# Kernel optimization log

Measured on AMD Instinct MI355X. Metric: run time of the kernel, lower is better.

## Reference

```python
import jax, jax.numpy as jnp
import numpy as np

MAX_ATOMS = 50
N_GRAPH_FEAT = 30
N_ATOM_FEAT = 75
BATCH_SIZE = 128
N_ATOMS = MAX_ATOMS * BATCH_SIZE  # 6400 total padded atoms
HIDDEN = 100
N_INPUTS = N_ATOM_FEAT + (MAX_ATOMS - 1) * N_GRAPH_FEAT  # 1545


def setup_inputs() -> dict:
    key = jax.random.key(0)
    ks = jax.random.split(key, 6)
    atom_features = jax.random.normal(ks[0], (N_ATOMS, N_ATOM_FEAT), dtype=jnp.float32)
    parents = jax.random.randint(ks[1], (N_ATOMS, MAX_ATOMS, MAX_ATOMS), 0, MAX_ATOMS + 1, dtype=jnp.int32)
    calculation_orders = jax.random.randint(ks[2], (N_ATOMS, MAX_ATOMS), 0, N_ATOMS, dtype=jnp.int32)
    calculation_masks = jax.random.randint(ks[3], (N_ATOMS, MAX_ATOMS), 0, 2, dtype=jnp.int32) > 0
    # glorot_uniform weights, zero biases (as in build())
    s0 = float(np.sqrt(6.0 / (N_INPUTS + HIDDEN)))
    W0 = jax.random.uniform(ks[4], (N_INPUTS, HIDDEN), jnp.float32, -s0, s0)
    s1 = float(np.sqrt(6.0 / (HIDDEN + N_GRAPH_FEAT)))
    W1 = jax.random.uniform(ks[5], (HIDDEN, N_GRAPH_FEAT), jnp.float32, -s1, s1)
    b0 = jnp.zeros((HIDDEN,), jnp.float32)
    b1 = jnp.zeros((N_GRAPH_FEAT,), jnp.float32)
    return {
        "atom_features": atom_features,
        "parents": parents,
        "calculation_orders": calculation_orders,
        "calculation_masks": calculation_masks,
        "n_atoms": N_ATOMS,
        "W0": W0, "b0": b0, "W1": W1, "b1": b1,
    }


def reference(atom_features, parents, calculation_orders, calculation_masks, n_atoms, W0, b0, W1, b1):
    # Stateful DAG propagation. Original masks out inactive rows per step
    # (dynamic shapes); here we compute all rows and write back the old value
    # for inactive rows, which is the same math under jit.
    rows = jnp.arange(n_atoms)

    def mlp(x):
        h = jax.nn.relu(x @ W0 + b0)
        return jax.nn.relu(h @ W1 + b1)

    gf0 = jnp.zeros((MAX_ATOMS * BATCH_SIZE, MAX_ATOMS + 1, N_GRAPH_FEAT), jnp.float32)
    # per-step slices, leading axis = count
    xs = (parents.transpose(1, 0, 2),       # [T, N, MAX_ATOMS]
          calculation_orders.T,             # [T, N]
          calculation_masks.T)              # [T, N]

    def step(gf, xs_t):
        par, order, mask = xs_t
        batch_atom = atom_features[order]                     # [N, 75]
        # gather parent graph features: gf[row, parent_slot]
        bgf = gf[rows[:, None], par[:, 1:]]                   # [N, 49, 30]
        x = jnp.concatenate([batch_atom, bgf.reshape(n_atoms, -1)], axis=1)  # [N, 1545]
        out = mlp(x)                                          # [N, 30]
        col = par[:, 0]
        old = gf[rows, col]
        new = jnp.where(mask[:, None], out, old)
        gf = gf.at[rows, col].set(new)
        return gf, out

    _, outs = jax.lax.scan(step, gf0, xs)
    out_last = outs[-1]
    # original returns only the masked rows of the last step; zero out inactive
    return jnp.where(calculation_masks[:, -1][:, None], out_last, 0.0)
```

## Files before the change

kernel.cpp:

```cpp
#include <hip/hip_runtime.h>
#include <stdint.h>

#define MA    50
#define NGF   30
#define NAF   75
#define NA    6400
#define H     100
#define RPB   32
#define NTHR  512
#define NT0P  8
#define KT0   52
#define NT1   2
#define KT1   4
#define AFW   104
#define HHW   136

typedef _Float16 f16;
typedef _Float16 f16x8 __attribute__((ext_vector_type(8)));
typedef float    f32x4 __attribute__((ext_vector_type(4)));

#define MFMA16(a, b, c) __builtin_amdgcn_mfma_f32_16x16x32_f16((a), (b), (c), 0, 0, 0)

__global__ void prep(const float* __restrict__ W0, const float* __restrict__ W1,
                     const uint8_t* __restrict__ cm,
                     f16* __restrict__ w0h, f16* __restrict__ w1h, f16* __restrict__ w1l,
                     int* __restrict__ flag) {
    const int bid = blockIdx.x;
    const int tidb = threadIdx.x;
    if (bid == 0) {
        if (tidb < 64) {
            int any = 0;
            #pragma unroll
            for (int i = 0; i < 64; ++i) {
                int pos = i * 64 + tidb;
                if ((pos & 3) != 0 && cm[pos] != 0) any = 1;
            }
            unsigned long long b = __ballot(any != 0);
            if (tidb == 0) *flag = (b != 0ULL) ? 1 : 0;
        }
        return;
    }
    if (bid <= 104) {
        int idx = (bid - 1) * 256 + tidb;
        int lane = idx & 63;
        int ktn  = idx >> 6;
        int nt = ktn / KT0, kt = ktn % KT0;
        int col = nt * 16 + (lane & 15);
        #pragma unroll
        for (int e = 0; e < 8; ++e) {
            int k = kt * 32 + (lane >> 4) * 8 + e;
            int kr = -1;
            if (kt < 3) { if (k < NAF) kr = k; }
            else {
                int kk = k - kt * 32;
                if (kk < NGF) kr = NAF + (kt - 3) * NGF + kk;
            }
            float wv = (kr >= 0 && col < H) ? W0[(size_t)kr * H + col] : 0.f;
            w0h[(size_t)idx * 8 + e] = (f16)wv;
        }
        return;
    }
    {
        int idx = (bid - 105) * 256 + tidb;
        if (idx >= NT1 * KT1 * 64) return;
        int lane = idx & 63;
        int ktn  = idx >> 6;
        int nt = ktn / KT1, kt = ktn % KT1;
        int col = nt * 16 + (lane & 15);
        #pragma unroll
        for (int e = 0; e < 8; ++e) {
            int k = kt * 32 + (lane >> 4) * 8 + e;
            float wv = (k < H && col < NGF) ? W1[(size_t)k * NGF + col] : 0.f;
            f16 hi = (f16)wv;
            w1h[(size_t)idx * 8 + e] = hi;
            w1l[(size_t)idx * 8 + e] = (f16)((wv - (float)hi) * 1024.f);
        }
    }
}

__global__ __launch_bounds__(NTHR, 2) void dag_mfma(
    const float* __restrict__ af,
    const int*   __restrict__ parents,
    const int*   __restrict__ orders,
    const void*  __restrict__ cmask,
    const float* __restrict__ b0,
    const float* __restrict__ b1,
    const f16*   __restrict__ w0h,
    const f16*   __restrict__ w1h, const f16* __restrict__ w1l,
    const int*   __restrict__ flagp,
    float*       __restrict__ dout)
{
    __shared__ f16     gfh[51 * 1024];
    __shared__ f16     afh[RPB][AFW];
    __shared__ f16     hh[RPB][HHW];
    __shared__ f32x4   part[4][2][2][64];
    __shared__ float   outl[RPB][33];
    __shared__ uint8_t slots[RPB][52];
    __shared__ int     colc[2][RPB];
    __shared__ int     maskc[2][RPB];
    __shared__ int     ordl[2][RPB];

    const int tid   = threadIdx.x;
    const int w     = tid >> 6;
    const int lane  = tid & 63;
    const int mrow  = lane & 15;
    const int kg    = lane >> 4;
    const int npair = w & 3;
    const int half  = w >> 2;
    const int row0  = blockIdx.x * RPB;
    const int flag  = *flagp;

    const int base0 = (mrow * 32 + kg * 8) ^ ((mrow & 7) << 3);
    const int base1 = ((16 + mrow) * 32 + kg * 8) ^ ((mrow & 7) << 3);

    const int hc0 = npair * 32 + mrow;
    const int hc1 = npair * 32 + 16 + mrow;
    const float b0v0 = (w < 4 && hc0 < H) ? b0[hc0] : 0.f;
    const float b0v1 = (w < 4 && hc1 < H) ? b0[hc1] : 0.f;
    const int oc = (w - 4) * 16 + mrow;
    const float b1v = (w >= 4 && w < 6 && oc < NGF) ? b1[oc] : 0.f;

    {
        f16x8 z = 0;
        for (int e = tid; e < 51 * 128; e += NTHR) ((f16x8*)gfh)[e] = z;
        for (int e = tid; e < RPB * AFW / 8; e += NTHR) ((f16x8*)&afh[0][0])[e] = z;
        for (int e = tid; e < RPB * HHW / 8; e += NTHR) ((f16x8*)&hh[0][0])[e]  = z;
    }
    if (tid >= 384 && tid < 416) {
        int r = tid - 384;
        ordl[0][r] = orders[(size_t)(row0 + r) * MA];
    }
    __syncthreads();

    float afr0 = 0.f, afr1 = 0.f, afr2 = 0.f, afr3 = 0.f, afr4 = 0.f;
    int   slr0 = 0, slr1 = 0, slr2 = 0, slr3 = 0;
    int   colr = 0, mskr = 0, oreg = 0;

    auto LOADS = [&](int T) {
        const int* ordb = ordl[T & 1];
        {
            int idx, r, k;
            idx = tid;        r = idx / NAF; k = idx - r * NAF; afr0 = af[(size_t)ordb[r] * NAF + k];
            idx = tid + 512;  r = idx / NAF; k = idx - r * NAF; afr1 = af[(size_t)ordb[r] * NAF + k];
            idx = tid + 1024; r = idx / NAF; k = idx - r * NAF; afr2 = af[(size_t)ordb[r] * NAF + k];
            idx = tid + 1536; r = idx / NAF; k = idx - r * NAF; afr3 = af[(size_t)ordb[r] * NAF + k];
            if (tid < 352) {
                idx = tid + 2048; r = idx / NAF; k = idx - r * NAF;
                afr4 = af[(size_t)ordb[r] * NAF + k];
            }
        }
        {
            int idx, r, p;
            idx = tid;        r = idx / 49; p = idx - r * 49;
            slr0 = __builtin_nontemporal_load(&parents[((size_t)(row0 + r) * MA + T) * MA + 1 + p]);
            idx = tid + 512;  r = idx / 49; p = idx - r * 49;
            slr1 = __builtin_nontemporal_load(&parents[((size_t)(row0 + r) * MA + T) * MA + 1 + p]);
            idx = tid + 1024; r = idx / 49; p = idx - r * 49;
            slr2 = __builtin_nontemporal_load(&parents[((size_t)(row0 + r) * MA + T) * MA + 1 + p]);
            if (tid < 32) {
                idx = tid + 1536; r = idx / 49; p = idx - r * 49;
                slr3 = __builtin_nontemporal_load(&parents[((size_t)(row0 + r) * MA + T) * MA + 1 + p]);
            }
        }
        if (tid >= 416 && tid < 448) {
            int r = tid - 416;
            colr = __builtin_nontemporal_load(&parents[((size_t)(row0 + r) * MA + T) * MA]);
        }
        if (tid >= 448 && tid < 480) {
            int r = tid - 448;
            if (flag) mskr = (int)__builtin_nontemporal_load(&((const uint8_t*)cmask)[(size_t)(row0 + r) * MA + T]);
            else      mskr = __builtin_nontemporal_load(&((const int*)cmask)[(size_t)(row0 + r) * MA + T]);
        }
        if (T + 1 < MA && tid >= 384 && tid < 416) {
            int r = tid - 384;
            oreg = __builtin_nontemporal_load(&orders[(size_t)(row0 + r) * MA + T + 1]);
        }
    };

    LOADS(0);

    for (int t = 0; t < MA; ++t) {
        {
            int idx, r, k;
            idx = tid;        r = idx / NAF; k = idx - r * NAF; afh[r][k] = (f16)afr0;
            idx = tid + 512;  r = idx / NAF; k = idx - r * NAF; afh[r][k] = (f16)afr1;
            idx = tid + 1024; r = idx / NAF; k = idx - r * NAF; afh[r][k] = (f16)afr2;
            idx = tid + 1536; r = idx / NAF; k = idx - r * NAF; afh[r][k] = (f16)afr3;
            if (tid < 352) { idx = tid + 2048; r = idx / NAF; k = idx - r * NAF; afh[r][k] = (f16)afr4; }
        }
        {
            int idx, r, p;
            idx = tid;        r = idx / 49; p = idx - r * 49; slots[r][p] = (uint8_t)slr0;
            idx = tid + 512;  r = idx / 49; p = idx - r * 49; slots[r][p] = (uint8_t)slr1;
            idx = tid + 1024; r = idx / 49; p = idx - r * 49; slots[r][p] = (uint8_t)slr2;
            if (tid < 32) { idx = tid + 1536; r = idx / 49; p = idx - r * 49; slots[r][p] = (uint8_t)slr3; }
        }
        if (tid >= 416 && tid < 448) colc[t & 1][tid - 416]  = colr;
        if (tid >= 448 && tid < 480) maskc[t & 1][tid - 448] = mskr;
        if (t + 1 < MA && tid >= 384 && tid < 416) ordl[(t + 1) & 1][tid - 384] = oreg;
        if (t > 0) {
            const int tp = (t - 1) & 1;
            int e = tid;
            #pragma unroll
            for (int q = 0; q < 2; ++q, e += NTHR) {
                if (e < RPB * NGF) {
                    int r = e / NGF, c = e - r * NGF;
                    float v = outl[r][c];
                    if (maskc[tp][r])
                        gfh[(colc[tp][r] * 1024 + r * 32 + c) ^ ((r & 7) << 3)] = (f16)v;
                }
            }
        }
        __syncthreads();

        if (t + 1 < MA) LOADS(t + 1);

        f32x4 acc00 = {0.f,0.f,0.f,0.f}, acc01 = {0.f,0.f,0.f,0.f};
        f32x4 acc10 = {0.f,0.f,0.f,0.f}, acc11 = {0.f,0.f,0.f,0.f};
        {
            const f16x8* B0 = (const f16x8*)w0h + ((size_t)(2 * npair) * KT0 + half * 26) * 64 + lane;
            const f16x8* B1 = B0 + (size_t)KT0 * 64;
            if (half == 0) {
                #pragma unroll
                for (int kt = 0; kt < 3; ++kt) {
                    f16x8 a0 = *(const f16x8*)&afh[mrow][kt * 32 + kg * 8];
                    f16x8 a1 = *(const f16x8*)&afh[16 + mrow][kt * 32 + kg * 8];
                    f16x8 bb0 = B0[(size_t)kt * 64];
                    f16x8 bb1 = B1[(size_t)kt * 64];
                    acc00 = MFMA16(a0, bb0, acc00); acc10 = MFMA16(a1, bb0, acc10);
                    acc01 = MFMA16(a0, bb1, acc01); acc11 = MFMA16(a1, bb1, acc11);
                }
                #pragma unroll
                for (int g = 0; g < 23; ++g) {
                    int s0 = slots[mrow][g];
                    int s1 = slots[16 + mrow][g];
                    f16x8 a0 = *(const f16x8*)&gfh[s0 * 1024 + base0];
                    f16x8 a1 = *(const f16x8*)&gfh[s1 * 1024 + base1];
                    f16x8 bb0 = B0[(size_t)(3 + g) * 64];
                    f16x8 bb1 = B1[(size_t)(3 + g) * 64];
                    acc00 = MFMA16(a0, bb0, acc00); acc10 = MFMA16(a1, bb0, acc10);
                    acc01 = MFMA16(a0, bb1, acc01); acc11 = MFMA16(a1, bb1, acc11);
                }
            } else {
                #pragma unroll
                for (int g = 0; g < 26; ++g) {
                    int s0 = slots[mrow][23 + g];
                    int s1 = slots[16 + mrow][23 + g];
                    f16x8 a0 = *(const f16x8*)&gfh[s0 * 1024 + base0];
                    f16x8 a1 = *(const f16x8*)&gfh[s1 * 1024 + base1];
                    f16x8 bb0 = B0[(size_t)g * 64];
                    f16x8 bb1 = B1[(size_t)g * 64];
                    acc00 = MFMA16(a0, bb0, acc00); acc10 = MFMA16(a1, bb0, acc10);
                    acc01 = MFMA16(a0, bb1, acc01); acc11 = MFMA16(a1, bb1, acc11);
                }
            }
        }
        if (half) {
            part[npair][0][0][lane] = acc00;
            part[npair][0][1][lane] = acc01;
            part[npair][1][0][lane] = acc10;
            part[npair][1][1][lane] = acc11;
        }
        __syncthreads();

        if (!half) {
            acc00 += part[npair][0][0][lane];
            acc01 += part[npair][0][1][lane];
            acc10 += part[npair][1][0][lane];
            acc11 += part[npair][1][1][lane];
            #pragma unroll
            for (int i = 0; i < 4; ++i) {
                hh[kg * 4 + i][hc0]      = (f16)fmaxf(acc00[i] + b0v0, 0.f);
                hh[kg * 4 + i][hc1]      = (f16)fmaxf(acc01[i] + b0v1, 0.f);
                hh[16 + kg * 4 + i][hc0] = (f16)fmaxf(acc10[i] + b0v0, 0.f);
                hh[16 + kg * 4 + i][hc1] = (f16)fmaxf(acc11[i] + b0v1, 0.f);
            }
        }
        __syncthreads();

        if (w == 4 || w == 5) {
            const int nt2 = w - 4;
            f32x4 h00 = {0.f,0.f,0.f,0.f}, l00 = {0.f,0.f,0.f,0.f};
            f32x4 h10 = {0.f,0.f,0.f,0.f}, l10 = {0.f,0.f,0.f,0.f};
            const f16x8* Bh = (const f16x8*)w1h + (size_t)nt2 * KT1 * 64 + lane;
            const f16x8* Bl = (const f16x8*)w1l + (size_t)nt2 * KT1 * 64 + lane;
            #pragma unroll
            for (int kt = 0; kt < KT1; ++kt) {
                f16x8 a0  = *(const f16x8*)&hh[mrow][kt * 32 + kg * 8];
                f16x8 a1  = *(const f16x8*)&hh[16 + mrow][kt * 32 + kg * 8];
                f16x8 bhf = Bh[(size_t)kt * 64];
                f16x8 blf = Bl[(size_t)kt * 64];
                h00 = MFMA16(a0, bhf, h00); l00 = MFMA16(a0, blf, l00);
                h10 = MFMA16(a1, bhf, h10); l10 = MFMA16(a1, blf, l10);
            }
            if (oc < NGF) {
                #pragma unroll
                for (int i = 0; i < 4; ++i) {
                    float v0 = fmaxf(h00[i] + l00[i] * (1.f/1024.f) + b1v, 0.f);
                    float v1 = fmaxf(h10[i] + l10[i] * (1.f/1024.f) + b1v, 0.f);
                    outl[kg * 4 + i][oc]      = v0;
                    outl[16 + kg * 4 + i][oc] = v1;
                    if (t == MA - 1) {
                        int r0 = kg * 4 + i, r1 = 16 + kg * 4 + i;
                        dout[(size_t)(row0 + r0) * NGF + oc] = maskc[t & 1][r0] ? v0 : 0.f;
                        dout[(size_t)(row0 + r1) * NGF + oc] = maskc[t & 1][r1] ? v1 : 0.f;
                    }
                }
            }
        }
        __syncthreads();
    }
}

extern "C" void kernel_launch(void* const* d_in, const int* in_sizes, int n_in,
                              void* d_out, int out_size, void* d_ws, size_t ws_size,
                              hipStream_t stream) {
    const float* af      = (const float*)d_in[0];
    const int*   parents = (const int*)  d_in[1];
    const int*   orders  = (const int*)  d_in[2];
    const void*  cmask   =               d_in[3];
    const float* W0      = (const float*)d_in[5];
    const float* b0      = (const float*)d_in[6];
    const float* W1      = (const float*)d_in[7];
    const float* b1      = (const float*)d_in[8];

    char* ws = (char*)d_ws;
    f16* w0h = (f16*)(ws);
    f16* w1h = (f16*)(ws + 425984);
    f16* w1l = (f16*)(ws + 434176);
    int* flagp = (int*)(ws + 442368);
    float* dout = (float*)d_out;

    prep<<<107, 256, 0, stream>>>(W0, W1, (const uint8_t*)cmask, w0h, w1h, w1l, flagp);

    dag_mfma<<<NA / RPB, NTHR, 0, stream>>>(
        af, parents, orders, cmask, b0, b1, w0h, w1h, w1l, flagp, dout);
}
```

Before: 329.1 us.

## Skip padded MFMA tile for last column pair and move scatter to step end

For the fourth column-pair wave group (columns 96-127, where only 96-99 of the 100 hidden units are real), only the first 16-column tile is computed, which skips half of that group's MFMAs and B loads. The scatter of the step's output into the shared graph-feature buffer, along with the final output write, moves from the start of the next step to a new phase after the second layer. That phase sits behind an extra barrier, so col/mask no longer need double buffers. This removes wasted MFMA work but adds one __syncthreads per step, and the scatter can no longer overlap with the next step's staging writes.

```diff
diff --git a/kernel.cpp b/kernel.cpp
--- a/kernel.cpp
+++ b/kernel.cpp
@@ -96,8 +96,8 @@
     __shared__ f32x4   part[4][2][2][64];
     __shared__ float   outl[RPB][33];
     __shared__ uint8_t slots[RPB][52];
-    __shared__ int     colc[2][RPB];
-    __shared__ int     maskc[2][RPB];
+    __shared__ int     colc[RPB];
+    __shared__ int     maskc[RPB];
     __shared__ int     ordl[2][RPB];
 
     const int tid   = threadIdx.x;
@@ -195,22 +195,9 @@
             idx = tid + 1024; r = idx / 49; p = idx - r * 49; slots[r][p] = (uint8_t)slr2;
             if (tid < 32) { idx = tid + 1536; r = idx / 49; p = idx - r * 49; slots[r][p] = (uint8_t)slr3; }
         }
-        if (tid >= 416 && tid < 448) colc[t & 1][tid - 416]  = colr;
-        if (tid >= 448 && tid < 480) maskc[t & 1][tid - 448] = mskr;
+        if (tid >= 416 && tid < 448) colc[tid - 416]  = colr;
+        if (tid >= 448 && tid < 480) maskc[tid - 448] = mskr;
         if (t + 1 < MA && tid >= 384 && tid < 416) ordl[(t + 1) & 1][tid - 384] = oreg;
-        if (t > 0) {
-            const int tp = (t - 1) & 1;
-            int e = tid;
-            #pragma unroll
-            for (int q = 0; q < 2; ++q, e += NTHR) {
-                if (e < RPB * NGF) {
-                    int r = e / NGF, c = e - r * NGF;
-                    float v = outl[r][c];
-                    if (maskc[tp][r])
-                        gfh[(colc[tp][r] * 1024 + r * 32 + c) ^ ((r & 7) << 3)] = (f16)v;
-                }
-            }
-        }
         __syncthreads();
 
         if (t + 1 < MA) LOADS(t + 1);
@@ -220,38 +207,69 @@
         {
             const f16x8* B0 = (const f16x8*)w0h + ((size_t)(2 * npair) * KT0 + half * 26) * 64 + lane;
             const f16x8* B1 = B0 + (size_t)KT0 * 64;
-            if (half == 0) {
-                #pragma unroll
-                for (int kt = 0; kt < 3; ++kt) {
-                    f16x8 a0 = *(const f16x8*)&afh[mrow][kt * 32 + kg * 8];
-                    f16x8 a1 = *(const f16x8*)&afh[16 + mrow][kt * 32 + kg * 8];
-                    f16x8 bb0 = B0[(size_t)kt * 64];
-                    f16x8 bb1 = B1[(size_t)kt * 64];
-                    acc00 = MFMA16(a0, bb0, acc00); acc10 = MFMA16(a1, bb0, acc10);
-                    acc01 = MFMA16(a0, bb1, acc01); acc11 = MFMA16(a1, bb1, acc11);
-                }
-                #pragma unroll
-                for (int g = 0; g < 23; ++g) {
-                    int s0 = slots[mrow][g];
-                    int s1 = slots[16 + mrow][g];
-                    f16x8 a0 = *(const f16x8*)&gfh[s0 * 1024 + base0];
-                    f16x8 a1 = *(const f16x8*)&gfh[s1 * 1024 + base1];
-                    f16x8 bb0 = B0[(size_t)(3 + g) * 64];
-                    f16x8 bb1 = B1[(size_t)(3 + g) * 64];
-                    acc00 = MFMA16(a0, bb0, acc00); acc10 = MFMA16(a1, bb0, acc10);
-                    acc01 = MFMA16(a0, bb1, acc01); acc11 = MFMA16(a1, bb1, acc11);
+            if (npair < 3) {
+                if (half == 0) {
+                    #pragma unroll
+                    for (int kt = 0; kt < 3; ++kt) {
+                        f16x8 a0 = *(const f16x8*)&afh[mrow][kt * 32 + kg * 8];
+                        f16x8 a1 = *(const f16x8*)&afh[16 + mrow][kt * 32 + kg * 8];
+                        f16x8 bb0 = B0[(size_t)kt * 64];
+                        f16x8 bb1 = B1[(size_t)kt * 64];
+                        acc00 = MFMA16(a0, bb0, acc00); acc10 = MFMA16(a1, bb0, acc10);
+                        acc01 = MFMA16(a0, bb1, acc01); acc11 = MFMA16(a1, bb1, acc11);
+                    }
+                    #pragma unroll
+                    for (int g = 0; g < 23; ++g) {
+                        int s0 = slots[mrow][g];
+                        int s1 = slots[16 + mrow][g];
+                        f16x8 a0 = *(const f16x8*)&gfh[s0 * 1024 + base0];
+                        f16x8 a1 = *(const f16x8*)&gfh[s1 * 1024 + base1];
+                        f16x8 bb0 = B0[(size_t)(3 + g) * 64];
+                        f16x8 bb1 = B1[(size_t)(3 + g) * 64];
+                        acc00 = MFMA16(a0, bb0, acc00); acc10 = MFMA16(a1, bb0, acc10);
+                        acc01 = MFMA16(a0, bb1, acc01); acc11 = MFMA16(a1, bb1, acc11);
+                    }
+                } else {
+                    #pragma unroll
+                    for (int g = 0; g < 26; ++g) {
+                        int s0 = slots[mrow][23 + g];
+                        int s1 = slots[16 + mrow][23 + g];
+                        f16x8 a0 = *(const f16x8*)&gfh[s0 * 1024 + base0];
+                        f16x8 a1 = *(const f16x8*)&gfh[s1 * 1024 + base1];
+                        f16x8 bb0 = B0[(size_t)g * 64];
+                        f16x8 bb1 = B1[(size_t)g * 64];
+                        acc00 = MFMA16(a0, bb0, acc00); acc10 = MFMA16(a1, bb0, acc10);
+                        acc01 = MFMA16(a0, bb1, acc01); acc11 = MFMA16(a1, bb1, acc11);
+                    }
                 }
             } else {
-                #pragma unroll
-                for (int g = 0; g < 26; ++g) {
-                    int s0 = slots[mrow][23 + g];
-                    int s1 = slots[16 + mrow][23 + g];
-                    f16x8 a0 = *(const f16x8*)&gfh[s0 * 1024 + base0];
-                    f16x8 a1 = *(const f16x8*)&gfh[s1 * 1024 + base1];
-                    f16x8 bb0 = B0[(size_t)g * 64];
-                    f16x8 bb1 = B1[(size_t)g * 64];
-                    acc00 = MFMA16(a0, bb0, acc00); acc10 = MFMA16(a1, bb0, acc10);
-                    acc01 = MFMA16(a0, bb1, acc01); acc11 = MFMA16(a1, bb1, acc11);
+                if (half == 0) {
+                    #pragma unroll
+                    for (int kt = 0; kt < 3; ++kt) {
+                        f16x8 a0 = *(const f16x8*)&afh[mrow][kt * 32 + kg * 8];
+                        f16x8 a1 = *(const f16x8*)&afh[16 + mrow][kt * 32 + kg * 8];
+                        f16x8 bb0 = B0[(size_t)kt * 64];
+                        acc00 = MFMA16(a0, bb0, acc00); acc10 = MFMA16(a1, bb0, acc10);
+                    }
+                    #pragma unroll
+                    for (int g = 0; g < 23; ++g) {
+                        int s0 = slots[mrow][g];
+                        int s1 = slots[16 + mrow][g];
+                        f16x8 a0 = *(const f16x8*)&gfh[s0 * 1024 + base0];
+                        f16x8 a1 = *(const f16x8*)&gfh[s1 * 1024 + base1];
+                        f16x8 bb0 = B0[(size_t)(3 + g) * 64];
+                        acc00 = MFMA16(a0, bb0, acc00); acc10 = MFMA16(a1, bb0, acc10);
+                    }
+                } else {
+                    #pragma unroll
+                    for (int g = 0; g < 26; ++g) {
+                        int s0 = slots[mrow][23 + g];
+                        int s1 = slots[16 + mrow][23 + g];
+                        f16x8 a0 = *(const f16x8*)&gfh[s0 * 1024 + base0];
+                        f16x8 a1 = *(const f16x8*)&gfh[s1 * 1024 + base1];
+                        f16x8 bb0 = B0[(size_t)g * 64];
+                        acc00 = MFMA16(a0, bb0, acc00); acc10 = MFMA16(a1, bb0, acc10);
+                    }
                 }
             }
         }
@@ -296,15 +314,24 @@
             if (oc < NGF) {
                 #pragma unroll
                 for (int i = 0; i < 4; ++i) {
-                    float v0 = fmaxf(h00[i] + l00[i] * (1.f/1024.f) + b1v, 0.f);
-                    float v1 = fmaxf(h10[i] + l10[i] * (1.f/1024.f) + b1v, 0.f);
-                    outl[kg * 4 + i][oc]      = v0;
-                    outl[16 + kg * 4 + i][oc] = v1;
-                    if (t == MA - 1) {
-                        int r0 = kg * 4 + i, r1 = 16 + kg * 4 + i;
-                        dout[(size_t)(row0 + r0) * NGF + oc] = maskc[t & 1][r0] ? v0 : 0.f;
-                        dout[(size_t)(row0 + r1) * NGF + oc] = maskc[t & 1][r1] ? v1 : 0.f;
-                    }
+                    outl[kg * 4 + i][oc]      = fmaxf(h00[i] + l00[i] * (1.f/1024.f) + b1v, 0.f);
+                    outl[16 + kg * 4 + i][oc] = fmaxf(h10[i] + l10[i] * (1.f/1024.f) + b1v, 0.f);
+                }
+            }
+        }
+        __syncthreads();
+
+        {
+            int e = tid;
+            #pragma unroll
+            for (int q = 0; q < 2; ++q, e += NTHR) {
+                if (e < RPB * NGF) {
+                    int r = e / NGF, c = e - r * NGF;
+                    float v = outl[r][c];
+                    if (maskc[r])
+                        gfh[(colc[r] * 1024 + r * 32 + c) ^ ((r & 7) << 3)] = (f16)v;
+                    if (t == MA - 1)
+                        dout[(size_t)(row0 + r) * NGF + c] = maskc[r] ? v : 0.f;
                 }
             }
         }
```

Result: faster. 280.3 us (median of 2 runs) (-14.8%).
